# Kernel tuning notes

Hardware: AMD Instinct MI355X
Metric: run time of the kernel (lower is better)

## Reference

```python
import jax, jax.numpy as jnp
import numpy as np

N_EMBD = 1024
HEAD_SIZE = 64

def setup_inputs() -> dict:
    key = jax.random.key(0)
    k1, k2, k3, k4 = jax.random.split(key, 4)
    x = jax.random.normal(k1, (8, 2048, N_EMBD), dtype=jnp.float32)
    s = 1.0 / np.sqrt(N_EMBD)
    Wk = jax.random.normal(k2, (HEAD_SIZE, N_EMBD), dtype=jnp.float32) * s
    Wq = jax.random.normal(k3, (HEAD_SIZE, N_EMBD), dtype=jnp.float32) * s
    Wv = jax.random.normal(k4, (HEAD_SIZE, N_EMBD), dtype=jnp.float32) * s
    return {"x": x, "Wk": Wk, "Wq": Wq, "Wv": Wv}

def reference(x, Wk, Wq, Wv):
    B, T, C = x.shape
    k = jnp.einsum('btc,hc->bth', x, Wk)  # [B,T,Hd]
    q = jnp.einsum('btc,hc->bth', x, Wq)
    v = jnp.einsum('btc,hc->bth', x, Wv)
    # NOTE: original scales by C**-0.5 where C = n_embd (not head_size)
    wei = jnp.einsum('bqh,bkh->bqk', q, k) * (C ** -0.5)  # [B,T,T]
    causal = jnp.tril(jnp.ones((T, T), dtype=bool))
    wei = jnp.where(causal, wei, -jnp.inf)
    wei = jax.nn.softmax(wei, axis=-1)
    out = jnp.einsum('bqk,bkh->bqh', wei, v)  # [B,T,Hd]
    return out
```

## Files before the change

kernel.cpp:

```cpp
#include <hip/hip_runtime.h>


typedef __attribute__((ext_vector_type(4))) short sv4;
typedef __attribute__((ext_vector_type(8))) short sv8;
typedef __attribute__((ext_vector_type(4))) float f32x4;

#define NB   8
#define TSEQ 2048
#define CDIM 1024
#define HD   64
#define MROWS (NB * TSEQ)

__device__ __forceinline__ short f2s(float f) {
  union { float f; unsigned u; } v; v.f = f;
  unsigned u = v.u;
  u += 0x7fffu + ((u >> 16) & 1u);
  return (short)(u >> 16);
}
__device__ __forceinline__ unsigned pk2(float lo, float hi) {
  return (unsigned)(unsigned short)f2s(lo) | ((unsigned)(unsigned short)f2s(hi) << 16);
}
__device__ __forceinline__ void glds16(const short* g, short* l) {
  __builtin_amdgcn_global_load_lds(
      (const __attribute__((address_space(1))) unsigned int*)g,
      (__attribute__((address_space(3))) unsigned int*)l, 16, 0, 0);
}

__global__ __launch_bounds__(256) void wcvt(
    const float* __restrict__ Wq, const float* __restrict__ Wk,
    const float* __restrict__ Wv, short* __restrict__ wb)
{
  int i = blockIdx.x * 256 + threadIdx.x;
  int t = i / 3072;
  int rem = i - t * 3072;
  int r = rem >> 4, s = rem & 15;
  int j = r >> 6, wrow = r & 63;
  const float* W = (j == 0) ? Wq : (j == 1) ? Wk : Wv;
  const float* src = W + (size_t)wrow * CDIM + t * 128 + ((s ^ (wrow & 7)) << 3);
  float4 a = *(const float4*)src;
  float4 b = *(const float4*)(src + 4);
  sv8 v = {f2s(a.x), f2s(a.y), f2s(a.z), f2s(a.w),
           f2s(b.x), f2s(b.y), f2s(b.z), f2s(b.w)};
  *(sv8*)(wb + (size_t)i * 8) = v;
}

__global__ __launch_bounds__(1024) void qkv_proj(
    const float* __restrict__ x,
    const short* __restrict__ wb,
    short* __restrict__ qw,
    short* __restrict__ kw,
    short* __restrict__ vtw)
{
  __shared__ short wlds[2][24576];
  __shared__ short xlds[2][8192];
  const int tid  = threadIdx.x;
  const int wid  = tid >> 6;
  const int lane = tid & 63;
  const int g    = lane >> 4;
  const int c16  = lane & 15;
  const int rowg = wid >> 2;
  const int ph   = wid & 3;
  const int row0 = blockIdx.x * 64;

  const int xr = tid >> 4, xs = tid & 15;
  const float* xsrc = x + (size_t)(row0 + xr) * CDIM + xs * 8;
  const int xwo = xr * 128 + ((xs ^ (xr & 7)) << 3);

  const int arow = rowg * 16 + c16;
  const int x7   = arow & 7;
  int rWo[3], rW7[3];
  #pragma unroll
  for (int p6 = 0; p6 < 3; ++p6) {
    int p = ph * 3 + p6;
    int r = (p >> 2) * 64 + (p & 3) * 16 + c16;
    rWo[p6] = r * 128;
    rW7[p6] = r & 7;
  }

  f32x4 acc[3];
  #pragma unroll
  for (int p6 = 0; p6 < 3; ++p6) acc[p6] = (f32x4){0.f, 0.f, 0.f, 0.f};

  float4 px[2][2];

  #pragma unroll
  for (int k2 = 0; k2 < 3; ++k2)
    glds16(wb + (size_t)(tid + k2 * 1024) * 8, &wlds[0][(tid + k2 * 1024) * 8]);
  px[0][0] = *(const float4*)(xsrc);
  px[0][1] = *(const float4*)(xsrc + 4);
  px[1][0] = *(const float4*)(xsrc + 128);
  px[1][1] = *(const float4*)(xsrc + 132);
  asm volatile("s_waitcnt vmcnt(2)" ::: "memory");
  {
    float4 A = px[0][0], B = px[0][1];
    sv8 v = {f2s(A.x), f2s(A.y), f2s(A.z), f2s(A.w),
             f2s(B.x), f2s(B.y), f2s(B.z), f2s(B.w)};
    *(sv8*)&xlds[0][xwo] = v;
  }
  asm volatile("s_waitcnt lgkmcnt(0)" ::: "memory");
  __builtin_amdgcn_sched_barrier(0);
  __builtin_amdgcn_s_barrier();

  #pragma unroll
  for (int t = 0; t < 8; ++t) {
    const int buf = t & 1;
    if (t < 7) {
      #pragma unroll
      for (int k2 = 0; k2 < 3; ++k2)
        glds16(wb + (size_t)((t + 1) * 3072 + tid + k2 * 1024) * 8,
               &wlds[buf ^ 1][(tid + k2 * 1024) * 8]);
    }
    if (t < 6) {
      px[t & 1][0] = *(const float4*)(xsrc + (t + 2) * 128);
      px[t & 1][1] = *(const float4*)(xsrc + (t + 2) * 128 + 4);
    }
    if (t < 7) {
      float4 A = px[(t + 1) & 1][0], B = px[(t + 1) & 1][1];
      sv8 v = {f2s(A.x), f2s(A.y), f2s(A.z), f2s(A.w),
               f2s(B.x), f2s(B.y), f2s(B.z), f2s(B.w)};
      *(sv8*)&xlds[buf ^ 1][xwo] = v;
    }
    #pragma unroll
    for (int kk = 0; kk < 4; ++kk) {
      int kslot = kk * 4 + g;
      sv8 a = *(const sv8*)&xlds[buf][arow * 128 + ((kslot ^ x7) << 3)];
      #pragma unroll
      for (int p6 = 0; p6 < 3; ++p6) {
        sv8 bfr = *(const sv8*)&wlds[buf][rWo[p6] + ((kslot ^ rW7[p6]) << 3)];
        acc[p6] = __builtin_amdgcn_mfma_f32_16x16x32_bf16(a, bfr, acc[p6], 0, 0, 0);
      }
    }
    if (t < 7) {
      if (t < 6) asm volatile("s_waitcnt vmcnt(2) lgkmcnt(0)" ::: "memory");
      else       asm volatile("s_waitcnt vmcnt(0) lgkmcnt(0)" ::: "memory");
      __builtin_amdgcn_sched_barrier(0);
      __builtin_amdgcn_s_barrier();
    }
  }

  #pragma unroll
  for (int p6 = 0; p6 < 3; ++p6) {
    int p = ph * 3 + p6, j = p >> 2, n = p & 3;
    #pragma unroll
    for (int r = 0; r < 4; ++r) {
      int rr = row0 + rowg * 16 + (g << 2) + r;
      int cc = (n << 4) + c16;
      if (j == 0) {
        qw[(size_t)rr * HD + cc] = f2s(acc[p6][r] * 0.03125f);
      } else if (j == 1) {
        kw[(size_t)rr * HD + ((((cc >> 3) ^ (rr & 7)) << 3) | (cc & 7))] =
            f2s(acc[p6][r]);
      } else {
        int b = rr >> 11, ti = rr & (TSEQ - 1);
        int kt = ti >> 6, key = ti & 63;
        vtw[(((size_t)b * 32 + kt) * 64 + cc) * 64 +
            ((((key >> 3) ^ (cc & 7)) << 3) | (key & 7))] = f2s(acc[p6][r]);
      }
    }
  }
}

__global__ __launch_bounds__(256) void attn(
    const short* __restrict__ qw,
    const short* __restrict__ kw,
    const short* __restrict__ vtw,
    float* __restrict__ Opart,
    float* __restrict__ mlws)
{
  __shared__ short kbuf[2][8192];
  __shared__ short vbuf[2][8192];
  __shared__ short bridge[4][2048];

  const int tid  = threadIdx.x;
  const int wid  = tid >> 6;
  const int lane = tid & 63;
  const int g    = lane >> 4;
  const int c16  = lane & 15;

  const int bid   = blockIdx.x;
  const int h     = bid >> 8;
  const int sub   = bid & 255;
  const int batch = sub & 7;
  const int jj    = sub >> 3;
  const int qb    = h ? (31 - jj) : jj;
  const int q0    = qb << 6;
  const size_t base = (size_t)batch * TSEQ * HD;

  const int ntot = (qb >> 1) + 1;
  const int th_  = (ntot + 1) >> 1;
  const int t0   = h ? th_ : 0;
  const int t1   = h ? ntot : th_;

  const int qrow = q0 + (wid << 4) + c16;
  sv8 qa0 = *(const sv8*)(qw + base + (size_t)qrow * HD + (g << 3));
  sv8 qa1 = *(const sv8*)(qw + base + (size_t)qrow * HD + 32 + (g << 3));

  float m = -1e30f, l = 0.f;
  f32x4 o[4];
  #pragma unroll
  for (int n = 0; n < 4; ++n) o[n] = (f32x4){0.f, 0.f, 0.f, 0.f};

  short* br = &bridge[wid][0];
  const int sx = c16 & 15;

  #define STAGE(tt, bb)                                                      \
    {                                                                        \
      const short* ksrc = kw + base + (size_t)(tt) * 8192;                   \
      const short* vsrc = vtw + ((size_t)batch * 32 + (tt) * 2) * 4096;      \
      _Pragma("unroll")                                                      \
      for (int q = 0; q < 4; ++q)                                            \
        glds16(ksrc + (tid + q * 256) * 8, &kbuf[bb][(tid + q * 256) * 8]);  \
      _Pragma("unroll")                                                      \
      for (int q = 0; q < 4; ++q)                                            \
        glds16(vsrc + (tid + q * 256) * 8, &vbuf[bb][(tid + q * 256) * 8]);  \
    }

  if (t0 < t1) {
    STAGE(t0, 0);
    asm volatile("s_waitcnt vmcnt(0)" ::: "memory");
    __builtin_amdgcn_s_barrier();

    for (int t = t0; t < t1; ++t) {
      const int buf = (t - t0) & 1;
      if (t + 1 < t1) STAGE(t + 1, buf ^ 1);

      f32x4 s[8];
      #pragma unroll
      for (int n = 0; n < 8; ++n) s[n] = (f32x4){0.f, 0.f, 0.f, 0.f};
      __builtin_amdgcn_s_setprio(1);
      #pragma unroll
      for (int n = 0; n < 8; ++n) {
        int kr = (n << 4) + c16;
        sv8 k0 = *(const sv8*)&kbuf[buf][kr * 64 + ((g ^ (kr & 7)) << 3)];
        s[n] = __builtin_amdgcn_mfma_f32_16x16x32_bf16(k0, qa0, s[n], 0, 0, 0);
        sv8 k1 = *(const sv8*)&kbuf[buf][kr * 64 + (((4 + g) ^ (kr & 7)) << 3)];
        s[n] = __builtin_amdgcn_mfma_f32_16x16x32_bf16(k1, qa1, s[n], 0, 0, 0);
      }
      __builtin_amdgcn_s_setprio(0);

      if (t == (qb >> 1)) {
        #pragma unroll
        for (int n = 0; n < 8; ++n) {
          int key = (t << 7) + (n << 4) + (g << 2);
          #pragma unroll
          for (int r = 0; r < 4; ++r)
            s[n][r] = (key + r <= qrow) ? s[n][r] : -1e30f;
        }
      }

      float mx = -1e30f;
      #pragma unroll
      for (int n = 0; n < 8; ++n)
        mx = fmaxf(mx, fmaxf(fmaxf(s[n][0], s[n][1]), fmaxf(s[n][2], s[n][3])));
      mx = fmaxf(mx, __shfl_xor(mx, 16));
      mx = fmaxf(mx, __shfl_xor(mx, 32));
      float mnew  = fmaxf(m, mx);
      float alpha = __expf(m - mnew);
      m = mnew;

      float sum = 0.f;
      #pragma unroll
      for (int n = 0; n < 8; ++n) {
        float p0 = __expf(s[n][0] - mnew);
        float p1 = __expf(s[n][1] - mnew);
        float p2 = __expf(s[n][2] - mnew);
        float p3 = __expf(s[n][3] - mnew);
        sum += (p0 + p1) + (p2 + p3);
        int slot = 2 * n + (g >> 1);
        uint2 w2; w2.x = pk2(p0, p1); w2.y = pk2(p2, p3);
        *(uint2*)&br[c16 * 128 + ((slot ^ sx) << 3) + ((g & 1) << 2)] = w2;
      }
      sum += __shfl_xor(sum, 16);
      sum += __shfl_xor(sum, 32);
      l = l * alpha + sum;

      float af[4];
      #pragma unroll
      for (int r = 0; r < 4; ++r) af[r] = __shfl(alpha, (g << 2) + r);
      #pragma unroll
      for (int n = 0; n < 4; ++n)
        #pragma unroll
        for (int r = 0; r < 4; ++r) o[n][r] *= af[r];

      asm volatile("s_waitcnt lgkmcnt(0)" ::: "memory");
      __builtin_amdgcn_sched_barrier(0);

      __builtin_amdgcn_s_setprio(1);
      #pragma unroll
      for (int kk = 0; kk < 4; ++kk) {
        int kslot = (kk << 2) + g;
        sv8 pa = *(const sv8*)&br[c16 * 128 + ((kslot ^ sx) << 3)];
        #pragma unroll
        for (int n = 0; n < 4; ++n) {
          int vr = (n << 4) + c16;
          sv8 vf = *(const sv8*)&vbuf[buf][(kslot >> 3) * 4096 + vr * 64 +
                                           (((kslot & 7) ^ (vr & 7)) << 3)];
          o[n] = __builtin_amdgcn_mfma_f32_16x16x32_bf16(pa, vf, o[n], 0, 0, 0);
        }
      }
      __builtin_amdgcn_s_setprio(0);

      if (t + 1 < t1) {
        asm volatile("s_waitcnt vmcnt(0)" ::: "memory");
        __builtin_amdgcn_sched_barrier(0);
        __builtin_amdgcn_s_barrier();
      }
    }
  }

  #pragma unroll
  for (int n = 0; n < 4; ++n) {
    #pragma unroll
    for (int r = 0; r < 4; ++r) {
      int row = (wid << 4) + (g << 2) + r;
      Opart[(size_t)bid * 4096 + row * 64 + (n << 4) + c16] = o[n][r];
    }
  }
  if (lane < 16) {
    int row = (wid << 4) + lane;
    mlws[((size_t)bid * 64 + row) * 2]     = m;
    mlws[((size_t)bid * 64 + row) * 2 + 1] = l;
  }
  #undef STAGE
}

__global__ __launch_bounds__(256) void combine(
    const float* __restrict__ Opart,
    const float* __restrict__ mlws,
    float* __restrict__ out)
{
  const int bid   = blockIdx.x;
  const int batch = bid & 7;
  const int qb    = bid >> 3;
  const int q0    = qb << 6;
  const int bid0  = bid;
  const int bid1  = 256 + ((31 - qb) << 3) + batch;

  const int tid = threadIdx.x;
  const int row = tid >> 2;
  const int cs  = (tid & 3) << 4;

  float m0 = mlws[((size_t)bid0 * 64 + row) * 2];
  float l0 = mlws[((size_t)bid0 * 64 + row) * 2 + 1];
  float m1 = mlws[((size_t)bid1 * 64 + row) * 2];
  float l1 = mlws[((size_t)bid1 * 64 + row) * 2 + 1];
  float M  = fmaxf(m0, m1);
  float a0 = __expf(m0 - M), a1 = __expf(m1 - M);
  float invL = 1.f / (l0 * a0 + l1 * a1);

  const float* O0 = Opart + (size_t)bid0 * 4096 + row * 64 + cs;
  const float* O1 = Opart + (size_t)bid1 * 4096 + row * 64 + cs;
  float* op = out + ((size_t)batch * TSEQ + q0 + row) * HD + cs;

  #pragma unroll
  for (int e = 0; e < 4; ++e) {
    float4 v0 = *(const float4*)(O0 + e * 4);
    float4 v1 = *(const float4*)(O1 + e * 4);
    float4 res;
    res.x = (v0.x * a0 + v1.x * a1) * invL;
    res.y = (v0.y * a0 + v1.y * a1) * invL;
    res.z = (v0.z * a0 + v1.z * a1) * invL;
    res.w = (v0.w * a0 + v1.w * a1) * invL;
    *(float4*)(op + e * 4) = res;
  }
}

extern "C" void kernel_launch(void* const* d_in, const int* in_sizes, int n_in,
                              void* d_out, int out_size, void* d_ws, size_t ws_size,
                              hipStream_t stream) {
  const float* x  = (const float*)d_in[0];
  const float* Wk = (const float*)d_in[1];
  const float* Wq = (const float*)d_in[2];
  const float* Wv = (const float*)d_in[3];
  float* out = (float*)d_out;

  short* qw  = (short*)d_ws;
  short* kw  = qw + (size_t)MROWS * HD;
  short* vtw = kw + (size_t)MROWS * HD;
  short* wb  = vtw + (size_t)NB * HD * TSEQ;
  float* Opart = (float*)(wb + 24576 * 8);
  float* mlws  = Opart + (size_t)512 * 4096;

  wcvt<<<dim3(96), dim3(256), 0, stream>>>(Wq, Wk, Wv, wb);
  qkv_proj<<<dim3(MROWS / 64), dim3(1024), 0, stream>>>(x, wb, qw, kw, vtw);
  attn<<<dim3(512), dim3(256), 0, stream>>>(qw, kw, vtw, Opart, mlws);
  combine<<<dim3(256), dim3(256), 0, stream>>>(Opart, mlws, out);
}
```

Measured before the change: 51.62 us.

## Restructure attention to 128-row query tiles with 4-way key split-K

The attention kernel now uses 512 threads (8 waves) per block, each block covering 128 query rows and a quarter of the causal key range, in place of 64-row tiles split two ways. The combine kernel merges four partial results per row instead of two. The P-to-LDS bridge is split into two halves so the PV MFMAs can start after half the probabilities are written. The V projection store is also vectorized to 4-wide writes. The aim is better balance and more reuse of K/V per block, at the cost of double-size partial buffers and a heavier combine step.

```diff
diff --git a/kernel.cpp b/kernel.cpp
--- a/kernel.cpp
+++ b/kernel.cpp
@@ -141,26 +141,30 @@
   #pragma unroll
   for (int p6 = 0; p6 < 3; ++p6) {
     int p = ph * 3 + p6, j = p >> 2, n = p & 3;
-    #pragma unroll
-    for (int r = 0; r < 4; ++r) {
-      int rr = row0 + rowg * 16 + (g << 2) + r;
-      int cc = (n << 4) + c16;
-      if (j == 0) {
-        qw[(size_t)rr * HD + cc] = f2s(acc[p6][r] * 0.03125f);
-      } else if (j == 1) {
-        kw[(size_t)rr * HD + ((((cc >> 3) ^ (rr & 7)) << 3) | (cc & 7))] =
-            f2s(acc[p6][r]);
-      } else {
-        int b = rr >> 11, ti = rr & (TSEQ - 1);
-        int kt = ti >> 6, key = ti & 63;
-        vtw[(((size_t)b * 32 + kt) * 64 + cc) * 64 +
-            ((((key >> 3) ^ (cc & 7)) << 3) | (key & 7))] = f2s(acc[p6][r]);
-      }
-    }
-  }
-}
-
-__global__ __launch_bounds__(256) void attn(
+    int cc  = (n << 4) + c16;
+    int rr0 = row0 + rowg * 16 + (g << 2);
+    if (j == 2) {
+      int b = rr0 >> 11, ti = rr0 & (TSEQ - 1);
+      int kt = ti >> 6, key = ti & 63;
+      sv4 v = {f2s(acc[p6][0]), f2s(acc[p6][1]), f2s(acc[p6][2]), f2s(acc[p6][3])};
+      *(sv4*)&vtw[(((size_t)b * 32 + kt) * 64 + cc) * 64 +
+                  ((((key >> 3) ^ (cc & 7)) << 3) | (key & 7))] = v;
+    } else {
+      #pragma unroll
+      for (int r = 0; r < 4; ++r) {
+        int rr = rr0 + r;
+        if (j == 0) {
+          qw[(size_t)rr * HD + cc] = f2s(acc[p6][r] * 0.03125f);
+        } else {
+          kw[(size_t)rr * HD + ((((cc >> 3) ^ (rr & 7)) << 3) | (cc & 7))] =
+              f2s(acc[p6][r]);
+        }
+      }
+    }
+  }
+}
+
+__global__ __launch_bounds__(512, 4) void attn(
     const short* __restrict__ qw,
     const short* __restrict__ kw,
     const short* __restrict__ vtw,
@@ -169,7 +173,7 @@
 {
   __shared__ short kbuf[2][8192];
   __shared__ short vbuf[2][8192];
-  __shared__ short bridge[4][2048];
+  __shared__ short bridge[8][1024];
 
   const int tid  = threadIdx.x;
   const int wid  = tid >> 6;
@@ -178,18 +182,15 @@
   const int c16  = lane & 15;
 
   const int bid   = blockIdx.x;
-  const int h     = bid >> 8;
-  const int sub   = bid & 255;
-  const int batch = sub & 7;
-  const int jj    = sub >> 3;
-  const int qb    = h ? (31 - jj) : jj;
-  const int q0    = qb << 6;
+  const int batch = bid & 7;
+  const int jb    = (bid >> 3) & 15;
+  const int qt    = bid >> 7;
+  const int q0    = jb << 7;
   const size_t base = (size_t)batch * TSEQ * HD;
 
-  const int ntot = (qb >> 1) + 1;
-  const int th_  = (ntot + 1) >> 1;
-  const int t0   = h ? th_ : 0;
-  const int t1   = h ? ntot : th_;
+  const int ntot = jb + 1;
+  const int t0   = (ntot * qt) >> 2;
+  const int t1   = (ntot * (qt + 1)) >> 2;
 
   const int qrow = q0 + (wid << 4) + c16;
   sv8 qa0 = *(const sv8*)(qw + base + (size_t)qrow * HD + (g << 3));
@@ -201,18 +202,16 @@
   for (int n = 0; n < 4; ++n) o[n] = (f32x4){0.f, 0.f, 0.f, 0.f};
 
   short* br = &bridge[wid][0];
-  const int sx = c16 & 15;
+  const int sx7 = c16 & 7;
 
   #define STAGE(tt, bb)                                                      \
     {                                                                        \
       const short* ksrc = kw + base + (size_t)(tt) * 8192;                   \
       const short* vsrc = vtw + ((size_t)batch * 32 + (tt) * 2) * 4096;      \
-      _Pragma("unroll")                                                      \
-      for (int q = 0; q < 4; ++q)                                            \
-        glds16(ksrc + (tid + q * 256) * 8, &kbuf[bb][(tid + q * 256) * 8]);  \
-      _Pragma("unroll")                                                      \
-      for (int q = 0; q < 4; ++q)                                            \
-        glds16(vsrc + (tid + q * 256) * 8, &vbuf[bb][(tid + q * 256) * 8]);  \
+      glds16(ksrc + tid * 8,         &kbuf[bb][tid * 8]);                    \
+      glds16(ksrc + (512 + tid) * 8, &kbuf[bb][(512 + tid) * 8]);            \
+      glds16(vsrc + tid * 8,         &vbuf[bb][tid * 8]);                    \
+      glds16(vsrc + (512 + tid) * 8, &vbuf[bb][(512 + tid) * 8]);            \
     }
 
   if (t0 < t1) {
@@ -238,7 +237,7 @@
       }
       __builtin_amdgcn_s_setprio(0);
 
-      if (t == (qb >> 1)) {
+      if (t == jb) {
         #pragma unroll
         for (int n = 0; n < 8; ++n) {
           int key = (t << 7) + (n << 4) + (g << 2);
@@ -265,10 +264,8 @@
         float p1 = __expf(s[n][1] - mnew);
         float p2 = __expf(s[n][2] - mnew);
         float p3 = __expf(s[n][3] - mnew);
+        s[n][0] = p0; s[n][1] = p1; s[n][2] = p2; s[n][3] = p3;
         sum += (p0 + p1) + (p2 + p3);
-        int slot = 2 * n + (g >> 1);
-        uint2 w2; w2.x = pk2(p0, p1); w2.y = pk2(p2, p3);
-        *(uint2*)&br[c16 * 128 + ((slot ^ sx) << 3) + ((g & 1) << 2)] = w2;
       }
       sum += __shfl_xor(sum, 16);
       sum += __shfl_xor(sum, 32);
@@ -282,23 +279,35 @@
         #pragma unroll
         for (int r = 0; r < 4; ++r) o[n][r] *= af[r];
 
-      asm volatile("s_waitcnt lgkmcnt(0)" ::: "memory");
-      __builtin_amdgcn_sched_barrier(0);
-
-      __builtin_amdgcn_s_setprio(1);
-      #pragma unroll
-      for (int kk = 0; kk < 4; ++kk) {
-        int kslot = (kk << 2) + g;
-        sv8 pa = *(const sv8*)&br[c16 * 128 + ((kslot ^ sx) << 3)];
+      #pragma unroll
+      for (int hv = 0; hv < 2; ++hv) {
         #pragma unroll
         for (int n = 0; n < 4; ++n) {
-          int vr = (n << 4) + c16;
-          sv8 vf = *(const sv8*)&vbuf[buf][(kslot >> 3) * 4096 + vr * 64 +
-                                           (((kslot & 7) ^ (vr & 7)) << 3)];
-          o[n] = __builtin_amdgcn_mfma_f32_16x16x32_bf16(pa, vf, o[n], 0, 0, 0);
+          int nn = (hv << 2) + n;
+          int slot = 2 * n + (g >> 1);
+          uint2 w2;
+          w2.x = pk2(s[nn][0], s[nn][1]);
+          w2.y = pk2(s[nn][2], s[nn][3]);
+          *(uint2*)&br[(c16 << 6) + ((slot ^ sx7) << 3) + ((g & 1) << 2)] = w2;
         }
-      }
-      __builtin_amdgcn_s_setprio(0);
+        asm volatile("s_waitcnt lgkmcnt(0)" ::: "memory");
+        __builtin_amdgcn_sched_barrier(0);
+        __builtin_amdgcn_s_setprio(1);
+        #pragma unroll
+        for (int kk = 0; kk < 2; ++kk) {
+          int kg    = (hv << 1) + kk;
+          int kslot = (kg << 2) + g;
+          sv8 pa = *(const sv8*)&br[(c16 << 6) + ((((kk << 2) + g) ^ sx7) << 3)];
+          #pragma unroll
+          for (int n = 0; n < 4; ++n) {
+            int vr = (n << 4) + c16;
+            sv8 vf = *(const sv8*)&vbuf[buf][(kslot >> 3) * 4096 + vr * 64 +
+                                             (((kslot & 7) ^ (vr & 7)) << 3)];
+            o[n] = __builtin_amdgcn_mfma_f32_16x16x32_bf16(pa, vf, o[n], 0, 0, 0);
+          }
+        }
+        __builtin_amdgcn_s_setprio(0);
+      }
 
       if (t + 1 < t1) {
         asm volatile("s_waitcnt vmcnt(0)" ::: "memory");
@@ -313,13 +322,13 @@
     #pragma unroll
     for (int r = 0; r < 4; ++r) {
       int row = (wid << 4) + (g << 2) + r;
-      Opart[(size_t)bid * 4096 + row * 64 + (n << 4) + c16] = o[n][r];
+      Opart[(size_t)bid * 8192 + row * 64 + (n << 4) + c16] = o[n][r];
     }
   }
   if (lane < 16) {
     int row = (wid << 4) + lane;
-    mlws[((size_t)bid * 64 + row) * 2]     = m;
-    mlws[((size_t)bid * 64 + row) * 2 + 1] = l;
+    mlws[((size_t)bid * 128 + row) * 2]     = m;
+    mlws[((size_t)bid * 128 + row) * 2 + 1] = l;
   }
   #undef STAGE
 }
@@ -331,37 +340,39 @@
 {
   const int bid   = blockIdx.x;
   const int batch = bid & 7;
-  const int qb    = bid >> 3;
-  const int q0    = qb << 6;
-  const int bid0  = bid;
-  const int bid1  = 256 + ((31 - qb) << 3) + batch;
-
-  const int tid = threadIdx.x;
-  const int row = tid >> 2;
-  const int cs  = (tid & 3) << 4;
-
-  float m0 = mlws[((size_t)bid0 * 64 + row) * 2];
-  float l0 = mlws[((size_t)bid0 * 64 + row) * 2 + 1];
-  float m1 = mlws[((size_t)bid1 * 64 + row) * 2];
-  float l1 = mlws[((size_t)bid1 * 64 + row) * 2 + 1];
-  float M  = fmaxf(m0, m1);
-  float a0 = __expf(m0 - M), a1 = __expf(m1 - M);
-  float invL = 1.f / (l0 * a0 + l1 * a1);
-
-  const float* O0 = Opart + (size_t)bid0 * 4096 + row * 64 + cs;
-  const float* O1 = Opart + (size_t)bid1 * 4096 + row * 64 + cs;
-  float* op = out + ((size_t)batch * TSEQ + q0 + row) * HD + cs;
-
+  const int jb    = (bid >> 3) & 15;
+  const int half  = bid >> 7;
+  const int tid   = threadIdx.x;
+  const int row   = (half << 6) + (tid >> 2);
+  const int cs    = (tid & 3) << 4;
+  const int pb0   = (jb << 3) + batch;
+
+  float mq[4], lq[4];
+  #pragma unroll
+  for (int q = 0; q < 4; ++q) {
+    int pb = (q << 7) + pb0;
+    mq[q] = mlws[((size_t)pb * 128 + row) * 2];
+    lq[q] = mlws[((size_t)pb * 128 + row) * 2 + 1];
+  }
+  float M = fmaxf(fmaxf(mq[0], mq[1]), fmaxf(mq[2], mq[3]));
+  float w[4], L = 0.f;
+  #pragma unroll
+  for (int q = 0; q < 4; ++q) { w[q] = __expf(mq[q] - M); L += w[q] * lq[q]; }
+  float invL = 1.f / L;
+
+  float* op = out + ((size_t)batch * TSEQ + (jb << 7) + row) * HD + cs;
   #pragma unroll
   for (int e = 0; e < 4; ++e) {
-    float4 v0 = *(const float4*)(O0 + e * 4);
-    float4 v1 = *(const float4*)(O1 + e * 4);
-    float4 res;
-    res.x = (v0.x * a0 + v1.x * a1) * invL;
-    res.y = (v0.y * a0 + v1.y * a1) * invL;
-    res.z = (v0.z * a0 + v1.z * a1) * invL;
-    res.w = (v0.w * a0 + v1.w * a1) * invL;
-    *(float4*)(op + e * 4) = res;
+    float4 acc = {0.f, 0.f, 0.f, 0.f};
+    #pragma unroll
+    for (int q = 0; q < 4; ++q) {
+      int pb = (q << 7) + pb0;
+      float4 v = *(const float4*)(Opart + (size_t)pb * 8192 + row * 64 + cs + e * 4);
+      acc.x += v.x * w[q]; acc.y += v.y * w[q];
+      acc.z += v.z * w[q]; acc.w += v.w * w[q];
+    }
+    acc.x *= invL; acc.y *= invL; acc.z *= invL; acc.w *= invL;
+    *(float4*)(op + e * 4) = acc;
   }
 }
 
@@ -379,10 +390,10 @@
   short* vtw = kw + (size_t)MROWS * HD;
   short* wb  = vtw + (size_t)NB * HD * TSEQ;
   float* Opart = (float*)(wb + 24576 * 8);
-  float* mlws  = Opart + (size_t)512 * 4096;
+  float* mlws  = Opart + (size_t)512 * 8192;
 
   wcvt<<<dim3(96), dim3(256), 0, stream>>>(Wq, Wk, Wv, wb);
   qkv_proj<<<dim3(MROWS / 64), dim3(1024), 0, stream>>>(x, wb, qw, kw, vtw);
-  attn<<<dim3(512), dim3(256), 0, stream>>>(qw, kw, vtw, Opart, mlws);
+  attn<<<dim3(512), dim3(512), 0, stream>>>(qw, kw, vtw, Opart, mlws);
   combine<<<dim3(256), dim3(256), 0, stream>>>(Opart, mlws, out);
 }
```

New measurement: 52.29 us. Within noise of the previous version (+1.3%).
